# Performance work log

Hardware: AMD Instinct MI355X
Metric: run time of the kernel (lower is better)

The kernel has to match this reference:

```python
import jax, jax.numpy as jnp
import numpy as np

N, XC, YC, H, W_ = 1024, 512, 256, 8, 8
HID = 512


def setup_inputs() -> dict:
    key = jax.random.key(0)
    k = jax.random.split(key, 6)
    x_samples = jax.random.normal(k[0], (N, XC, H, W_), dtype=jnp.float32)
    y_samples = jax.random.normal(k[1], (N, YC, H, W_), dtype=jnp.float32)
    # p_mu: Linear(x_dim, hidden) -> ReLU -> Linear(hidden, y_dim)
    s1 = 1.0 / np.sqrt(XC)
    s2 = 1.0 / np.sqrt(HID)
    W1 = jax.random.uniform(k[2], (XC, HID), jnp.float32, -s1, s1)
    b1 = jax.random.uniform(k[3], (HID,), jnp.float32, -s1, s1)
    W2 = jax.random.uniform(k[4], (HID, YC), jnp.float32, -s2, s2)
    b2 = jax.random.uniform(k[5], (YC,), jnp.float32, -s2, s2)
    return {"x_samples": x_samples, "y_samples": y_samples,
            "W1": W1, "b1": b1, "W2": W2, "b2": b2}


def reference(x_samples, y_samples, W1, b1, W2, b2):
    # AdaptiveAvgPool2d(1) + flatten(1) == mean over spatial dims
    x_vec = x_samples.mean(axis=(2, 3))  # (N, x_dim)
    y_vec = y_samples.mean(axis=(2, 3))  # (N, y_dim)
    # p_mu MLP
    h = jax.nn.relu(x_vec @ W1 + b1)
    mu = h @ W2 + b2  # (N, y_dim)
    # positive: -(mu_i - y_i)^2 / 2, summed over D
    positive = (-((mu - y_vec) ** 2) / 2.0).sum(axis=-1)  # (N,)
    # negative: for each i, mean_j (y_j - mu_i)^2 / 2, summed over D
    diff = y_vec[None, :, :] - mu[:, None, :]  # (N, N, D)
    negative = (-(diff ** 2).mean(axis=1) / 2.0).sum(axis=-1)  # (N,)
    return (positive - negative).mean()
```

## Files before the change

kernel.cpp:

```cpp
#include <hip/hip_runtime.h>

#define N_SAMP 1024
#define XC_DIM 512
#define YC_DIM 256
#define HID_DIM 512

__global__ __launch_bounds__(256) void pool_kernel(
    const float* __restrict__ x, const float* __restrict__ y,
    float* __restrict__ x_vec, float* __restrict__ y_vec) {
  __shared__ float s[16 * 33];
  const int t = threadIdx.x;
  const long blk = blockIdx.x;
  const float4* src;
  float* dst;
  long obase;
  if (blk < 16384) {
    src = (const float4*)x; dst = x_vec; obase = blk * 32;
  } else {
    src = (const float4*)y; dst = y_vec; obase = (blk - 16384) * 32;
  }
  const float4* p = src + obase * 16;

  float4 v0 = p[t];
  float4 v1 = p[t + 256];
  float h0 = (v0.x + v0.y) + (v0.z + v0.w);
  float h1 = (v1.x + v1.y) + (v1.z + v1.w);

  s[(t & 15) * 33 + (t >> 4)] = h0;
  s[(t & 15) * 33 + 16 + (t >> 4)] = h1;
  __syncthreads();

  const int o = t >> 3;
  const int r = t & 7;
  float dp = s[(2 * r) * 33 + o] + s[(2 * r + 1) * 33 + o];
#pragma unroll
  for (int off = 1; off < 8; off <<= 1) dp += __shfl_xor(dp, off);
  if (r == 0) dst[obase + o] = dp * (1.0f / 64.0f);
}

#define TBK 16

__global__ __launch_bounds__(256) void gemm1_kernel(
    const float* __restrict__ A, const float* __restrict__ B,
    float* __restrict__ Hp) {
  const int K = 512, Nn = 512;
  __shared__ float As[TBK][68];
  __shared__ float Bs[TBK][68];
  const int t = threadIdx.x;
  const int bn = blockIdx.x * 64;
  const int bm = blockIdx.y * 64;
  const int ks = blockIdx.z;

  const int arow = t >> 2, acol = (t & 3) * 4;
  const int brow = t >> 4, bcol = (t & 15) * 4;
  const int row0 = (t >> 4) * 4, col0 = (t & 15) * 4;

  float acc[4][4] = {};
  const int k0 = ks * 128;

  float4 av = *(const float4*)&A[(bm + arow) * K + k0 + acol];
  float4 bv = *(const float4*)&B[(k0 + brow) * Nn + bn + bcol];

  for (int it = 0; it < 8; ++it) {
    __syncthreads();
    As[acol + 0][arow] = av.x;
    As[acol + 1][arow] = av.y;
    As[acol + 2][arow] = av.z;
    As[acol + 3][arow] = av.w;
    *(float4*)&Bs[brow][bcol] = bv;
    __syncthreads();
    if (it < 7) {
      const int k1 = k0 + (it + 1) * TBK;
      av = *(const float4*)&A[(bm + arow) * K + k1 + acol];
      bv = *(const float4*)&B[(k1 + brow) * Nn + bn + bcol];
    }
#pragma unroll
    for (int kk = 0; kk < TBK; ++kk) {
      float4 a = *(const float4*)&As[kk][row0];
      float4 b = *(const float4*)&Bs[kk][col0];
      acc[0][0] += a.x * b.x; acc[0][1] += a.x * b.y; acc[0][2] += a.x * b.z; acc[0][3] += a.x * b.w;
      acc[1][0] += a.y * b.x; acc[1][1] += a.y * b.y; acc[1][2] += a.y * b.z; acc[1][3] += a.y * b.w;
      acc[2][0] += a.z * b.x; acc[2][1] += a.z * b.y; acc[2][2] += a.z * b.z; acc[2][3] += a.z * b.w;
      acc[3][0] += a.w * b.x; acc[3][1] += a.w * b.y; acc[3][2] += a.w * b.z; acc[3][3] += a.w * b.w;
    }
  }

  float* H = Hp + (long)ks * (N_SAMP * HID_DIM);
#pragma unroll
  for (int i = 0; i < 4; ++i) {
    float4 o;
    o.x = acc[i][0]; o.y = acc[i][1]; o.z = acc[i][2]; o.w = acc[i][3];
    *(float4*)&H[(long)(bm + row0 + i) * Nn + bn + col0] = o;
  }
}

__global__ __launch_bounds__(256) void gemm2_kernel(
    const float* __restrict__ Hp, const float* __restrict__ b1,
    const float* __restrict__ B, float* __restrict__ Mup) {
  const int K = 512, Nn = 256;
  __shared__ float As[TBK][68];
  __shared__ float Bs[TBK][68];
  const int t = threadIdx.x;
  const int bn = blockIdx.x * 64;
  const int bm = blockIdx.y * 64;
  const int ks = blockIdx.z;
  const long HS = (long)N_SAMP * HID_DIM;

  const int arow = t >> 2, acol = (t & 3) * 4;
  const int brow = t >> 4, bcol = (t & 15) * 4;
  const int row0 = (t >> 4) * 4, col0 = (t & 15) * 4;

  float acc[4][4] = {};
  const int k0 = ks * 64;

  long aidx = (long)(bm + arow) * K + k0 + acol;
  float4 a0 = *(const float4*)&Hp[aidx];
  float4 a1 = *(const float4*)&Hp[aidx + HS];
  float4 a2 = *(const float4*)&Hp[aidx + 2 * HS];
  float4 a3 = *(const float4*)&Hp[aidx + 3 * HS];
  float4 bb = *(const float4*)&b1[k0 + acol];
  float4 bv = *(const float4*)&B[(k0 + brow) * Nn + bn + bcol];

  for (int it = 0; it < 4; ++it) {
    float4 av;
    av.x = fmaxf(a0.x + a1.x + a2.x + a3.x + bb.x, 0.0f);
    av.y = fmaxf(a0.y + a1.y + a2.y + a3.y + bb.y, 0.0f);
    av.z = fmaxf(a0.z + a1.z + a2.z + a3.z + bb.z, 0.0f);
    av.w = fmaxf(a0.w + a1.w + a2.w + a3.w + bb.w, 0.0f);
    __syncthreads();
    As[acol + 0][arow] = av.x;
    As[acol + 1][arow] = av.y;
    As[acol + 2][arow] = av.z;
    As[acol + 3][arow] = av.w;
    *(float4*)&Bs[brow][bcol] = bv;
    __syncthreads();
    if (it < 3) {
      const int k1 = k0 + (it + 1) * TBK;
      aidx = (long)(bm + arow) * K + k1 + acol;
      a0 = *(const float4*)&Hp[aidx];
      a1 = *(const float4*)&Hp[aidx + HS];
      a2 = *(const float4*)&Hp[aidx + 2 * HS];
      a3 = *(const float4*)&Hp[aidx + 3 * HS];
      bb = *(const float4*)&b1[k1 + acol];
      bv = *(const float4*)&B[(k1 + brow) * Nn + bn + bcol];
    }
#pragma unroll
    for (int kk = 0; kk < TBK; ++kk) {
      float4 a = *(const float4*)&As[kk][row0];
      float4 b = *(const float4*)&Bs[kk][col0];
      acc[0][0] += a.x * b.x; acc[0][1] += a.x * b.y; acc[0][2] += a.x * b.z; acc[0][3] += a.x * b.w;
      acc[1][0] += a.y * b.x; acc[1][1] += a.y * b.y; acc[1][2] += a.y * b.z; acc[1][3] += a.y * b.w;
      acc[2][0] += a.z * b.x; acc[2][1] += a.z * b.y; acc[2][2] += a.z * b.z; acc[2][3] += a.z * b.w;
      acc[3][0] += a.w * b.x; acc[3][1] += a.w * b.y; acc[3][2] += a.w * b.z; acc[3][3] += a.w * b.w;
    }
  }

  float* M = Mup + (long)ks * (N_SAMP * YC_DIM);
#pragma unroll
  for (int i = 0; i < 4; ++i) {
    float4 o;
    o.x = acc[i][0]; o.y = acc[i][1]; o.z = acc[i][2]; o.w = acc[i][3];
    *(float4*)&M[(long)(bm + row0 + i) * Nn + bn + col0] = o;
  }
}

__global__ __launch_bounds__(256) void reduce_kernel(
    const float* __restrict__ Mup, const float* __restrict__ b2,
    const float* __restrict__ yv, float* __restrict__ colsum_mu,
    float* __restrict__ colsum_y, float* __restrict__ dot_out) {
  const int d = threadIdx.x;
  const int n0 = blockIdx.x * 4;
  const long MS = (long)N_SAMP * YC_DIM;
  const float bb = b2[d];
  float cm = 0.f, cy = 0.f, dp = 0.f;
#pragma unroll
  for (int r = 0; r < 4; ++r) {
    const long idx = (long)(n0 + r) * YC_DIM + d;
    float mu = bb;
#pragma unroll
    for (int s = 0; s < 8; ++s) mu += Mup[idx + s * MS];
    const float yy = yv[idx];
    dp += mu * yy;
    cm += mu;
    cy += yy;
  }
  atomicAdd(&colsum_mu[d], cm);
  atomicAdd(&colsum_y[d], cy);
#pragma unroll
  for (int off = 1; off < 64; off <<= 1) dp += __shfl_xor(dp, off);
  if ((d & 63) == 0) atomicAdd(dot_out, dp);
}

__global__ __launch_bounds__(256) void finalize_kernel(
    const float* __restrict__ colsum_mu, const float* __restrict__ colsum_y,
    const float* __restrict__ dot_in, float* __restrict__ out) {
  __shared__ float partial[4];
  const int t = threadIdx.x;
  float v = colsum_mu[t] * colsum_y[t];
#pragma unroll
  for (int off = 1; off < 64; off <<= 1) v += __shfl_xor(v, off);
  if ((t & 63) == 0) partial[t >> 6] = v;
  __syncthreads();
  if (t == 0) {
    float tot = partial[0] + partial[1] + partial[2] + partial[3];
    out[0] = dot_in[0] * (1.0f / 1024.0f) - tot * (1.0f / (1024.0f * 1024.0f));
  }
}

extern "C" void kernel_launch(void* const* d_in, const int* in_sizes, int n_in,
                              void* d_out, int out_size, void* d_ws, size_t ws_size,
                              hipStream_t stream) {
  const float* x  = (const float*)d_in[0];
  const float* y  = (const float*)d_in[1];
  const float* W1 = (const float*)d_in[2];
  const float* b1 = (const float*)d_in[3];
  const float* W2 = (const float*)d_in[4];
  const float* b2 = (const float*)d_in[5];
  float* out = (float*)d_out;

  char* ws = (char*)d_ws;
  float* x_vec = (float*)ws;
  float* y_vec = (float*)(ws + (2lu << 20));
  float* Hp    = (float*)(ws + (4lu << 20));
  float* Mup   = (float*)(ws + (12lu << 20));
  float* accum = (float*)(ws + (20lu << 20));
  float* colsum_mu = accum;
  float* colsum_y  = accum + 256;
  float* dotp      = accum + 512;

  hipMemsetAsync(accum, 0, 513 * sizeof(float), stream);

  pool_kernel<<<24576, 256, 0, stream>>>(x, y, x_vec, y_vec);

  gemm1_kernel<<<dim3(8, 16, 4), 256, 0, stream>>>(x_vec, W1, Hp);

  gemm2_kernel<<<dim3(4, 16, 8), 256, 0, stream>>>(Hp, b1, W2, Mup);

  reduce_kernel<<<256, 256, 0, stream>>>(Mup, b2, y_vec, colsum_mu,
                                         colsum_y, dotp);

  finalize_kernel<<<1, 256, 0, stream>>>(colsum_mu, colsum_y, dotp, out);
}
```

Before: 277.5 us.

## Fuse column-sum and dot reductions into gemm2 epilogue, drop reduce kernel

The gemm2 epilogue now computes per-block partial column sums of mu, column sums of y, and the mu·y dot product directly from accumulator registers. These partials are written to small buffers instead of storing the full split-K Mup tensor. This removes the Mup write and read, the separate reduce kernel, the memset and the atomics. The b2 bias contribution is folded algebraically into finalize, which now reduces 128 partial rows serially in a single block.

```diff
diff --git a/kernel.cpp b/kernel.cpp
--- a/kernel.cpp
+++ b/kernel.cpp
@@ -96,10 +96,13 @@
 
 __global__ __launch_bounds__(256) void gemm2_kernel(
     const float* __restrict__ Hp, const float* __restrict__ b1,
-    const float* __restrict__ B, float* __restrict__ Mup) {
+    const float* __restrict__ B, const float* __restrict__ yv,
+    float* __restrict__ cs_part, float* __restrict__ ycs_part,
+    float* __restrict__ dot_part) {
   const int K = 512, Nn = 256;
   __shared__ float As[TBK][68];
   __shared__ float Bs[TBK][68];
+  __shared__ float redd[4];
   const int t = threadIdx.x;
   const int bn = blockIdx.x * 64;
   const int bm = blockIdx.y * 64;
@@ -155,55 +158,80 @@
     }
   }
 
-  float* M = Mup + (long)ks * (N_SAMP * YC_DIM);
+  float dp = 0.f;
+  float cmu0 = 0.f, cmu1 = 0.f, cmu2 = 0.f, cmu3 = 0.f;
+  float cy0 = 0.f, cy1 = 0.f, cy2 = 0.f, cy3 = 0.f;
 #pragma unroll
   for (int i = 0; i < 4; ++i) {
-    float4 o;
-    o.x = acc[i][0]; o.y = acc[i][1]; o.z = acc[i][2]; o.w = acc[i][3];
-    *(float4*)&M[(long)(bm + row0 + i) * Nn + bn + col0] = o;
-  }
-}
-
-__global__ __launch_bounds__(256) void reduce_kernel(
-    const float* __restrict__ Mup, const float* __restrict__ b2,
-    const float* __restrict__ yv, float* __restrict__ colsum_mu,
-    float* __restrict__ colsum_y, float* __restrict__ dot_out) {
-  const int d = threadIdx.x;
-  const int n0 = blockIdx.x * 4;
-  const long MS = (long)N_SAMP * YC_DIM;
-  const float bb = b2[d];
-  float cm = 0.f, cy = 0.f, dp = 0.f;
-#pragma unroll
-  for (int r = 0; r < 4; ++r) {
-    const long idx = (long)(n0 + r) * YC_DIM + d;
-    float mu = bb;
-#pragma unroll
-    for (int s = 0; s < 8; ++s) mu += Mup[idx + s * MS];
-    const float yy = yv[idx];
-    dp += mu * yy;
-    cm += mu;
-    cy += yy;
-  }
-  atomicAdd(&colsum_mu[d], cm);
-  atomicAdd(&colsum_y[d], cy);
+    const float4 yy = *(const float4*)&yv[(long)(bm + row0 + i) * Nn + bn + col0];
+    dp += acc[i][0] * yy.x + acc[i][1] * yy.y + acc[i][2] * yy.z + acc[i][3] * yy.w;
+    cmu0 += acc[i][0]; cmu1 += acc[i][1]; cmu2 += acc[i][2]; cmu3 += acc[i][3];
+    cy0 += yy.x; cy1 += yy.y; cy2 += yy.z; cy3 += yy.w;
+  }
 #pragma unroll
   for (int off = 1; off < 64; off <<= 1) dp += __shfl_xor(dp, off);
-  if ((d & 63) == 0) atomicAdd(dot_out, dp);
+
+  __syncthreads();
+  {
+    float4 o; o.x = cmu0; o.y = cmu1; o.z = cmu2; o.w = cmu3;
+    *(float4*)&As[t >> 4][col0] = o;
+    float4 q; q.x = cy0; q.y = cy1; q.z = cy2; q.w = cy3;
+    *(float4*)&Bs[t >> 4][col0] = q;
+  }
+  if ((t & 63) == 0) redd[t >> 6] = dp;
+  __syncthreads();
+
+  const int bid = blockIdx.x + 4 * blockIdx.y + 64 * blockIdx.z;
+  if (t < 64) {
+    float s = 0.f;
+#pragma unroll
+    for (int g = 0; g < 16; ++g) s += As[g][t];
+    cs_part[(blockIdx.y * 8 + ks) * 256 + bn + t] = s;
+  } else if (t < 128) {
+    if (ks == 0) {
+      const int c = t - 64;
+      float s = 0.f;
+#pragma unroll
+      for (int g = 0; g < 16; ++g) s += Bs[g][c];
+      ycs_part[blockIdx.y * 256 + bn + c] = s;
+    }
+  } else if (t == 128) {
+    dot_part[bid] = redd[0] + redd[1] + redd[2] + redd[3];
+  }
 }
 
 __global__ __launch_bounds__(256) void finalize_kernel(
-    const float* __restrict__ colsum_mu, const float* __restrict__ colsum_y,
-    const float* __restrict__ dot_in, float* __restrict__ out) {
-  __shared__ float partial[4];
-  const int t = threadIdx.x;
-  float v = colsum_mu[t] * colsum_y[t];
-#pragma unroll
-  for (int off = 1; off < 64; off <<= 1) v += __shfl_xor(v, off);
-  if ((t & 63) == 0) partial[t >> 6] = v;
+    const float* __restrict__ cs_part, const float* __restrict__ ycs_part,
+    const float* __restrict__ dot_part, const float* __restrict__ b2,
+    float* __restrict__ out) {
+  __shared__ float red[3][4];
+  const int t = threadIdx.x;
+  const float b2d = b2[t];
+  float cm = 1024.0f * b2d;
+#pragma unroll 8
+  for (int p = 0; p < 128; ++p) cm += cs_part[p * 256 + t];
+  float cy = 0.f;
+#pragma unroll
+  for (int p = 0; p < 16; ++p) cy += ycs_part[p * 256 + t];
+  float v1 = cm * cy;
+  float v2 = b2d * cy;
+  float v3 = dot_part[t] + dot_part[t + 256];
+#pragma unroll
+  for (int off = 1; off < 64; off <<= 1) {
+    v1 += __shfl_xor(v1, off);
+    v2 += __shfl_xor(v2, off);
+    v3 += __shfl_xor(v3, off);
+  }
+  if ((t & 63) == 0) {
+    red[0][t >> 6] = v1; red[1][t >> 6] = v2; red[2][t >> 6] = v3;
+  }
   __syncthreads();
   if (t == 0) {
-    float tot = partial[0] + partial[1] + partial[2] + partial[3];
-    out[0] = dot_in[0] * (1.0f / 1024.0f) - tot * (1.0f / (1024.0f * 1024.0f));
+    float S1 = red[0][0] + red[0][1] + red[0][2] + red[0][3];
+    float S2 = red[1][0] + red[1][1] + red[1][2] + red[1][3];
+    float S0 = red[2][0] + red[2][1] + red[2][2] + red[2][3];
+    float dot = S0 + S2;
+    out[0] = dot * (1.0f / 1024.0f) - S1 * (1.0f / (1024.0f * 1024.0f));
   }
 }
 
@@ -222,22 +250,16 @@
   float* x_vec = (float*)ws;
   float* y_vec = (float*)(ws + (2lu << 20));
   float* Hp    = (float*)(ws + (4lu << 20));
-  float* Mup   = (float*)(ws + (12lu << 20));
-  float* accum = (float*)(ws + (20lu << 20));
-  float* colsum_mu = accum;
-  float* colsum_y  = accum + 256;
-  float* dotp      = accum + 512;
-
-  hipMemsetAsync(accum, 0, 513 * sizeof(float), stream);
+  float* cs_part  = (float*)(ws + (12lu << 20));
+  float* ycs_part = (float*)(ws + (12lu << 20) + (160lu << 10));
+  float* dot_part = (float*)(ws + (12lu << 20) + (192lu << 10));
 
   pool_kernel<<<24576, 256, 0, stream>>>(x, y, x_vec, y_vec);
 
   gemm1_kernel<<<dim3(8, 16, 4), 256, 0, stream>>>(x_vec, W1, Hp);
 
-  gemm2_kernel<<<dim3(4, 16, 8), 256, 0, stream>>>(Hp, b1, W2, Mup);
-
-  reduce_kernel<<<256, 256, 0, stream>>>(Mup, b2, y_vec, colsum_mu,
-                                         colsum_y, dotp);
-
-  finalize_kernel<<<1, 256, 0, stream>>>(colsum_mu, colsum_y, dotp, out);
-}
+  gemm2_kernel<<<dim3(4, 16, 8), 256, 0, stream>>>(Hp, b1, W2, y_vec,
+                                                   cs_part, ycs_part, dot_part);
+
+  finalize_kernel<<<1, 256, 0, stream>>>(cs_part, ycs_part, dot_part, b2, out);
+}
```

New measurement: 261.3 us. -5.8%, faster.
